# Kernel optimization log

Hardware: AMD Instinct MI355X
Metric: run time of the kernel (lower is better)

The kernel has to match this reference:

```python
import jax, jax.numpy as jnp
import numpy as np

B, CIN, H, W = 4, 128, 128, 128
CH = CIN // 2          # channels after transpose conv (= 64)
COUT = 64
N2 = (B * 2 * H * 2 * W) // 2  # active sites of x2 (half of fine grid)


def setup_inputs() -> dict:
    key = jax.random.key(0)
    ks = jax.random.split(key, 8)
    n = lambda k, s, sc=1.0: jax.random.normal(k, s, jnp.float32) * sc
    return {
        "x1": n(ks[0], (B, CIN, H, W)),
        "x2_feat": n(ks[1], (N2, CH)),
        "w_up": n(ks[2], (CIN, CH, 2, 2), 0.05),   # torch ConvTranspose2d layout [in, out, kh, kw]
        "b_up": n(ks[3], (CH,), 0.05),
        "w1": n(ks[4], (CH, CH, 3, 3), 0.05),      # torch Conv2d layout [out, in, kh, kw]
        "b1": n(ks[5], (CH,), 0.05),
        "a1": jnp.full((1,), 0.25, jnp.float32),   # nn.PReLU default init
        "w2": n(ks[6], (COUT, CH, 3, 3), 0.05),
        "b2": n(ks[7], (COUT,), 0.05),
        "a2": jnp.full((1,), 0.25, jnp.float32),
    }


def _prelu(x, a):
    return jnp.where(x >= 0, x, a * x)


def _conv3(x, w, b):
    y = jax.lax.conv_general_dilated(x, w, (1, 1), 'SAME',
                                     dimension_numbers=('NCHW', 'OIHW', 'NCHW'))
    return y + b[None, :, None, None]


def reference(x1, x2_feat, w_up, b_up, w1, b1, a1, w2, b2, a2):
    Bn, _, Hn, Wn = x1.shape
    # ConvTranspose2d k=2, s=2 (non-overlapping) as an einsum:
    # up[b,o,2i+p,2j+q] = sum_c x1[b,c,i,j] * w_up[c,o,p,q]
    up = jnp.einsum('bchw,copq->bohpwq', x1, w_up).reshape(Bn, CH, 2 * Hn, 2 * Wn)
    up = up + b_up[None, :, None, None]
    # addspvec: larger tensor keeps its indices; first len(b) feature rows
    # are overwritten by the smaller tensor's features (spconv raster order).
    f = jnp.transpose(up, (0, 2, 3, 1)).reshape(-1, CH)  # [B*2H*2W, CH]
    f = f.at[:x2_feat.shape[0]].set(x2_feat)
    merged = jnp.transpose(f.reshape(Bn, 2 * Hn, 2 * Wn, CH), (0, 3, 1, 2))
    # DoubleConv: (SparseConv2d 3x3 pad1 -> PReLU) x 2 (dense-equivalent)
    h = _prelu(_conv3(merged, w1, b1), a1[0])
    out = _prelu(_conv3(h, w2, b2), a2[0])
    return out
```

## Files before the change

### kernel.cpp

```cpp
#include <hip/hip_runtime.h>

typedef __attribute__((ext_vector_type(8))) short short8;
typedef __attribute__((ext_vector_type(4))) float f32x4;

#define HF 256
#define WF 256

typedef const __attribute__((address_space(1))) void gbl_void;
typedef __attribute__((address_space(3))) void lds_void;

__device__ __forceinline__ ushort f2bf(float f) {
    uint u = __builtin_bit_cast(uint, f);
    u = (u + 0x7FFFu + ((u >> 16) & 1u)) >> 16;
    return (ushort)u;
}
__device__ __forceinline__ uint pack2(float a, float b) {
    return (uint)f2bf(a) | ((uint)f2bf(b) << 16);
}
__device__ __forceinline__ float prelu(float v, float al) { return v >= 0.f ? v : al * v; }

__global__ __launch_bounds__(256) void k_wprep(const float* __restrict__ w1,
                                               const float* __restrict__ w2,
                                               const float* __restrict__ wup,
                                               ushort* __restrict__ wT1,
                                               ushort* __restrict__ wT2,
                                               ushort* __restrict__ wupT,
                                               uint4* __restrict__ zeroBuf) {
    int idx = blockIdx.x * 256 + threadIdx.x;
    if (blockIdx.x == 0 && threadIdx.x < 16)
        zeroBuf[threadIdx.x] = make_uint4(0u, 0u, 0u, 0u);
    if (idx < 36864) {
        int tap = idx >> 12;
        int oc  = idx & 4095;
        int src = oc * 9 + tap;
        wT1[idx] = f2bf(w1[src]);
        wT2[idx] = f2bf(w2[src]);
    }
    if (idx < 32768) {
        int out = idx >> 7;
        int c   = idx & 127;
        int k   = out >> 6;
        int o   = out & 63;
        wupT[idx] = f2bf(wup[c * 256 + o * 4 + k]);
    }
}

__global__ __launch_bounds__(512) void k_upsample_mfma(const float* __restrict__ x1,
                                                       const ushort* __restrict__ wupT,
                                                       const float* __restrict__ bup,
                                                       ushort* __restrict__ upB) {
    __shared__ __align__(16) char lds[81920];

    const int t   = threadIdx.x;
    const int l   = t & 63;
    const int l15 = l & 15;
    const int l4  = l >> 4;
    const int w   = t >> 6;
    const int pg  = w & 3;
    const int oh  = w >> 2;
    const int i   = blockIdx.x >> 1;
    const int j0  = (blockIdx.x & 1) * 64;
    const int z   = blockIdx.y;
    const int gb  = 2 + z;

    {
        const int j  = t & 63;
        const int cg = t >> 6;
        const size_t base = ((size_t)gb * 128) * 16384 + (size_t)i * 128 + j0 + j;
        float xv[16];
#pragma unroll
        for (int r = 0; r < 2; ++r)
#pragma unroll
            for (int cc = 0; cc < 8; ++cc)
                xv[r * 8 + cc] = x1[base + (size_t)(cg * 16 + r * 8 + cc) * 16384];
#pragma unroll
        for (int r = 0; r < 2; ++r) {
            short8 pk;
#pragma unroll
            for (int cc = 0; cc < 8; ++cc) pk[cc] = (short)f2bf(xv[r * 8 + cc]);
            int ad = (j * 256 + (cg * 16 + r * 8) * 2) ^ ((j & 15) << 4);
            *(short8*)(lds + ad) = pk;
        }
    }
    {
        const uint4* src = (const uint4*)wupT;
#pragma unroll
        for (int rep = 0; rep < 8; ++rep) {
            int q   = rep * 512 + t;
            int out = q >> 4, c16 = q & 15;
            int ad  = 16384 + ((out * 256 + c16 * 16) ^ ((out & 15) << 4));
            *(uint4*)(lds + ad) = src[q];
        }
    }
    float bvv[4];
#pragma unroll
    for (int ob = 0; ob < 4; ++ob) bvv[ob] = bup[ob * 16 + l15];
    __syncthreads();

    f32x4 acc[2][4];
#pragma unroll
    for (int kk = 0; kk < 2; ++kk)
#pragma unroll
        for (int ob = 0; ob < 4; ++ob) acc[kk][ob] = (f32x4){0.f, 0.f, 0.f, 0.f};

#pragma unroll
    for (int ks = 0; ks < 4; ++ks) {
        const int cb = ks * 64 + (l4 << 4);
        const int rowA = pg * 16 + l15;
        short8 xfr = *(const short8*)(lds + ((rowA * 256 + cb) ^ ((rowA & 15) << 4)));
#pragma unroll
        for (int kk = 0; kk < 2; ++kk)
#pragma unroll
            for (int ob = 0; ob < 4; ++ob) {
                int out = (oh * 2 + kk) * 64 + ob * 16 + l15;
                short8 wfr = *(const short8*)(lds + 16384 +
                              ((out * 256 + cb) ^ ((out & 15) << 4)));
                acc[kk][ob] = __builtin_amdgcn_mfma_f32_16x16x32_bf16(xfr, wfr, acc[kk][ob], 0, 0, 0);
            }
    }
    __syncthreads();

    ushort* OUT = (ushort*)lds;
#pragma unroll
    for (int kk = 0; kk < 2; ++kk) {
        const int k = oh * 2 + kk, p = k >> 1, q = k & 1;
#pragma unroll
        for (int ob = 0; ob < 4; ++ob) {
            const int o = ob * 16 + l15;
#pragma unroll
            for (int r = 0; r < 4; ++r) {
                int jl = pg * 16 + l4 * 4 + r;
                int x  = 2 * jl + q;
                OUT[(p * 128 + x) * 64 + o] = f2bf(acc[kk][ob][r] + bvv[ob]);
            }
        }
    }
    __syncthreads();

#pragma unroll
    for (int rep = 0; rep < 4; ++rep) {
        int idx = rep * 512 + t;
        int p   = idx >> 10;
        int y   = 2 * i + p;
        uint4 v = *(const uint4*)(lds + idx * 16);
        size_t g = (size_t)(z * HF + y) * 2048 + (size_t)j0 * 16 + (idx & 1023);
        ((uint4*)upB)[g] = v;
    }
}

template<int IN_MODE, int OUT_NHWC>
__global__ __launch_bounds__(1024, 1) void k_conv(const float* __restrict__ x2,
                                                  const ushort* __restrict__ upB,
                                                  const ushort* __restrict__ inB,
                                                  const ushort* __restrict__ wT,
                                                  const float* __restrict__ bias,
                                                  const float* __restrict__ alpha,
                                                  const uint4* __restrict__ zeroBuf,
                                                  ushort* __restrict__ outB,
                                                  float* __restrict__ outF) {
    __shared__ __align__(16) ushort inL[5120 * 8];
    __shared__ __align__(16) ushort wL[9 * 64 * 64];

    const int t   = threadIdx.x;
    const int wv  = t >> 6;
    const int l   = t & 63;
    const int l15 = l & 15;
    const int l4  = l >> 4;
    const int x0  = (blockIdx.x & 7) * 32;
    const int y0  = (blockIdx.x >> 3) * 16;
    const int b   = blockIdx.y;

    {
        const char* wTb = (const char*)wT;
#pragma unroll
        for (int rep = 0; rep < 4; ++rep) {
            int d   = rep * 1024 + t;
            int tap = d >> 9;
            int dp  = d & 511;
            int s   = (tap << 9) + (dp ^ ((dp >> 3) & 7));
            __builtin_amdgcn_global_load_lds(
                (gbl_void*)(wTb + (size_t)s * 16),
                (lds_void*)((char*)wL + (size_t)((rep << 10) + (wv << 6)) * 16),
                16, 0, 0);
        }
        if (wv < 8) {
            int d   = 4096 + (wv << 6) + l;
            int tap = d >> 9;
            int dp  = d & 511;
            int s   = (tap << 9) + (dp ^ ((dp >> 3) & 7));
            __builtin_amdgcn_global_load_lds(
                (gbl_void*)(wTb + (size_t)s * 16),
                (lds_void*)((char*)wL + (size_t)(4096 + (wv << 6)) * 16),
                16, 0, 0);
        }
    }

    if (IN_MODE == 1 || b >= 2) {
        const ushort* src0 = (IN_MODE == 1) ? inB : upB;
        const int bb = (IN_MODE == 1) ? b : (b - 2);
#pragma unroll
        for (int rep = 0; rep < 5; ++rep) {
            int d  = rep * 1024 + t;
            int r  = d / 272;
            int wi = d - r * 272;
            int wq = wi ^ ((wi >> 3) & 7);
            int x  = wq >> 3, c8 = wq & 7;
            int gy = y0 - 1 + r;
            int gx = x0 - 1 + x;
            const void* g;
            if (d < 4896 && (unsigned)gy < HF && (unsigned)gx < WF) {
                size_t pos = (size_t)(bb * HF + gy) * WF + gx;
                g = (const void*)(src0 + pos * 64 + c8 * 8);
            } else {
                g = (const void*)zeroBuf;
            }
            __builtin_amdgcn_global_load_lds(
                (gbl_void*)g,
                (lds_void*)((char*)inL + (size_t)((rep << 10) + (wv << 6)) * 16),
                16, 0, 0);
        }
    } else {
        for (int q = t; q < 18 * 34 * 8; q += 1024) {
            int r   = q / 272;
            int rem = q - r * 272;
            int x   = rem >> 3;
            int c8  = rem & 7;
            int gy = y0 - 1 + r;
            int gx = x0 - 1 + x;
            uint4 v = make_uint4(0u, 0u, 0u, 0u);
            if ((unsigned)gy < HF && (unsigned)gx < WF) {
                size_t pos = (size_t)(b * HF + gy) * WF + gx;
                const float4* s = (const float4*)(x2 + pos * 64 + c8 * 8);
                float4 u0 = s[0], u1 = s[1];
                v = make_uint4(pack2(u0.x, u0.y), pack2(u0.z, u0.w),
                               pack2(u1.x, u1.y), pack2(u1.z, u1.w));
            }
            int ad = (q * 16) ^ ((x & 7) << 4);
            *(uint4*)((char*)inL + ad) = v;
        }
    }
    __syncthreads();

    f32x4 acc[2][4];
#pragma unroll
    for (int m = 0; m < 2; ++m)
#pragma unroll
        for (int nf = 0; nf < 4; ++nf) acc[m][nf] = (f32x4){0.f, 0.f, 0.f, 0.f};

#pragma unroll 1
    for (int tap = 0; tap < 9; ++tap) {
        const int ky = tap / 3;
        const int kx = tap - ky * 3;
        const char* wPage = (const char*)wL + tap * 8192;
#pragma unroll
        for (int ks = 0; ks < 2; ++ks) {
            short8 wfr[4];
#pragma unroll
            for (int nf = 0; nf < 4; ++nf) {
                int o = nf * 16 + l15;
                int ad = (o * 128 + ks * 64 + (l4 << 4)) ^ ((o & 7) << 4);
                wfr[nf] = *(const short8*)(wPage + ad);
            }
#pragma unroll
            for (int m = 0; m < 2; ++m) {
                int ry = wv + ky;
                int xl = m * 16 + l15 + kx;
                int ad = ((ry * 34 + xl) * 128 + ks * 64 + (l4 << 4)) ^ ((xl & 7) << 4);
                short8 ifr = *(const short8*)((const char*)inL + ad);
#pragma unroll
                for (int nf = 0; nf < 4; ++nf) {
                    if (OUT_NHWC)
                        acc[m][nf] = __builtin_amdgcn_mfma_f32_16x16x32_bf16(
                            wfr[nf], ifr, acc[m][nf], 0, 0, 0);
                    else
                        acc[m][nf] = __builtin_amdgcn_mfma_f32_16x16x32_bf16(
                            ifr, wfr[nf], acc[m][nf], 0, 0, 0);
                }
            }
        }
    }

    const float al = alpha[0];
    const int y = y0 + wv;
    if (OUT_NHWC) {
        float4 bv[4];
#pragma unroll
        for (int nf = 0; nf < 4; ++nf) bv[nf] = *(const float4*)(bias + nf * 16 + (l4 << 2));
#pragma unroll
        for (int m = 0; m < 2; ++m) {
            int x = x0 + m * 16 + l15;
#pragma unroll
            for (int nf = 0; nf < 4; ++nf) {
                f32x4 v = acc[m][nf];
                uint lo = pack2(prelu(v.x + bv[nf].x, al), prelu(v.y + bv[nf].y, al));
                uint hi = pack2(prelu(v.z + bv[nf].z, al), prelu(v.w + bv[nf].w, al));
                int cb = nf * 16 + (l4 << 2);
                *(uint2*)(outB + ((size_t)(b * HF + y) * WF + x) * 64 + cb) = make_uint2(lo, hi);
            }
        }
    } else {
        float bb[4];
#pragma unroll
        for (int nf = 0; nf < 4; ++nf) bb[nf] = bias[nf * 16 + l15];
#pragma unroll
        for (int m = 0; m < 2; ++m) {
            int xb = x0 + m * 16 + (l4 << 2);
#pragma unroll
            for (int nf = 0; nf < 4; ++nf) {
                f32x4 v = acc[m][nf];
                int cout = nf * 16 + l15;
                float4 st;
                st.x = prelu(v.x + bb[nf], al);
                st.y = prelu(v.y + bb[nf], al);
                st.z = prelu(v.z + bb[nf], al);
                st.w = prelu(v.w + bb[nf], al);
                *(float4*)(outF + (((size_t)b * 64 + cout) << 16) + y * WF + xb) = st;
            }
        }
    }
}

extern "C" void kernel_launch(void* const* d_in, const int* in_sizes, int n_in,
                              void* d_out, int out_size, void* d_ws, size_t ws_size,
                              hipStream_t stream) {
    const float* x1  = (const float*)d_in[0];
    const float* x2  = (const float*)d_in[1];
    const float* wup = (const float*)d_in[2];
    const float* bup = (const float*)d_in[3];
    const float* w1  = (const float*)d_in[4];
    const float* b1  = (const float*)d_in[5];
    const float* a1  = (const float*)d_in[6];
    const float* w2  = (const float*)d_in[7];
    const float* b2  = (const float*)d_in[8];
    const float* a2  = (const float*)d_in[9];

    char* ws = (char*)d_ws;
    ushort* upB  = (ushort*)ws;
    ushort* hB   = (ushort*)(ws + (size_t)(16 << 20));
    ushort* wT1  = (ushort*)(ws + (size_t)(48 << 20));
    ushort* wT2  = wT1 + 9 * 64 * 64;
    ushort* wupT = wT2 + 9 * 64 * 64;
    uint4*  zeroBuf = (uint4*)(ws + (size_t)(49 << 20));
    float* out = (float*)d_out;

    k_wprep<<<144, 256, 0, stream>>>(w1, w2, wup, wT1, wT2, wupT, zeroBuf);
    k_upsample_mfma<<<dim3(256, 2), 512, 0, stream>>>(x1, wupT, bup, upB);
    k_conv<0, 1><<<dim3(128, 4), 1024, 0, stream>>>(x2, upB, nullptr, wT1, b1, a1, zeroBuf, hB, nullptr);
    k_conv<1, 0><<<dim3(128, 4), 1024, 0, stream>>>(nullptr, nullptr, hB, wT2, b2, a2, zeroBuf, nullptr, out);
}
```

Baseline: 80.10 us.

## Split conv K dimension across wave halves with LDS reduction

```diff
diff --git a/kernel.cpp b/kernel.cpp
--- a/kernel.cpp
+++ b/kernel.cpp
@@ -158,11 +158,15 @@
                                                   const uint4* __restrict__ zeroBuf,
                                                   ushort* __restrict__ outB,
                                                   float* __restrict__ outF) {
-    __shared__ __align__(16) ushort inL[5120 * 8];
-    __shared__ __align__(16) ushort wL[9 * 64 * 64];
+    __shared__ __align__(16) char ldsAll[155648];
+    ushort* inL = (ushort*)ldsAll;
+    ushort* wL  = (ushort*)(ldsAll + 81920);
+    float*  redL = (float*)ldsAll;
 
     const int t   = threadIdx.x;
     const int wv  = t >> 6;
+    const int wk  = wv & 7;
+    const int ks  = wv >> 3;
     const int l   = t & 63;
     const int l15 = l & 15;
     const int l4  = l >> 4;
@@ -241,80 +245,100 @@
     }
     __syncthreads();
 
-    f32x4 acc[2][4];
-#pragma unroll
-    for (int m = 0; m < 2; ++m)
+    f32x4 acc[4][4];
+#pragma unroll
+    for (int m = 0; m < 4; ++m)
 #pragma unroll
         for (int nf = 0; nf < 4; ++nf) acc[m][nf] = (f32x4){0.f, 0.f, 0.f, 0.f};
+
+    const int ksb = ks * 64 + (l4 << 4);
 
 #pragma unroll 1
     for (int tap = 0; tap < 9; ++tap) {
         const int ky = tap / 3;
         const int kx = tap - ky * 3;
         const char* wPage = (const char*)wL + tap * 8192;
-#pragma unroll
-        for (int ks = 0; ks < 2; ++ks) {
-            short8 wfr[4];
+        short8 wfr[4];
+#pragma unroll
+        for (int nf = 0; nf < 4; ++nf) {
+            int o = nf * 16 + l15;
+            int ad = (o * 128 + ksb) ^ ((o & 7) << 4);
+            wfr[nf] = *(const short8*)(wPage + ad);
+        }
+#pragma unroll
+        for (int m = 0; m < 4; ++m) {
+            int ry = wk * 2 + (m >> 1) + ky;
+            int xl = (m & 1) * 16 + l15 + kx;
+            int ad = ((ry * 34 + xl) * 128 + ksb) ^ ((xl & 7) << 4);
+            short8 ifr = *(const short8*)((const char*)inL + ad);
 #pragma unroll
             for (int nf = 0; nf < 4; ++nf) {
-                int o = nf * 16 + l15;
-                int ad = (o * 128 + ks * 64 + (l4 << 4)) ^ ((o & 7) << 4);
-                wfr[nf] = *(const short8*)(wPage + ad);
-            }
-#pragma unroll
-            for (int m = 0; m < 2; ++m) {
-                int ry = wv + ky;
-                int xl = m * 16 + l15 + kx;
-                int ad = ((ry * 34 + xl) * 128 + ks * 64 + (l4 << 4)) ^ ((xl & 7) << 4);
-                short8 ifr = *(const short8*)((const char*)inL + ad);
+                if (OUT_NHWC)
+                    acc[m][nf] = __builtin_amdgcn_mfma_f32_16x16x32_bf16(
+                        wfr[nf], ifr, acc[m][nf], 0, 0, 0);
+                else
+                    acc[m][nf] = __builtin_amdgcn_mfma_f32_16x16x32_bf16(
+                        ifr, wfr[nf], acc[m][nf], 0, 0, 0);
+            }
+        }
+    }
+
+    __syncthreads();
+    if (ks == 1) {
+#pragma unroll
+        for (int m = 0; m < 4; ++m)
+#pragma unroll
+            for (int nf = 0; nf < 4; ++nf)
+                *(f32x4*)(redL + (size_t)(((wk * 16 + m * 4 + nf) * 64 + l) * 4)) = acc[m][nf];
+    }
+    __syncthreads();
+    if (ks == 0) {
+        const float al = alpha[0];
+#pragma unroll
+        for (int m = 0; m < 4; ++m)
+#pragma unroll
+            for (int nf = 0; nf < 4; ++nf) {
+                f32x4 p = *(const f32x4*)(redL + (size_t)(((wk * 16 + m * 4 + nf) * 64 + l) * 4));
+                acc[m][nf].x += p.x; acc[m][nf].y += p.y;
+                acc[m][nf].z += p.z; acc[m][nf].w += p.w;
+            }
+        if (OUT_NHWC) {
+            float4 bv[4];
+#pragma unroll
+            for (int nf = 0; nf < 4; ++nf) bv[nf] = *(const float4*)(bias + nf * 16 + (l4 << 2));
+#pragma unroll
+            for (int m = 0; m < 4; ++m) {
+                int y = y0 + wk * 2 + (m >> 1);
+                int x = x0 + (m & 1) * 16 + l15;
 #pragma unroll
                 for (int nf = 0; nf < 4; ++nf) {
-                    if (OUT_NHWC)
-                        acc[m][nf] = __builtin_amdgcn_mfma_f32_16x16x32_bf16(
-                            wfr[nf], ifr, acc[m][nf], 0, 0, 0);
-                    else
-                        acc[m][nf] = __builtin_amdgcn_mfma_f32_16x16x32_bf16(
-                            ifr, wfr[nf], acc[m][nf], 0, 0, 0);
+                    f32x4 v = acc[m][nf];
+                    uint lo = pack2(prelu(v.x + bv[nf].x, al), prelu(v.y + bv[nf].y, al));
+                    uint hi = pack2(prelu(v.z + bv[nf].z, al), prelu(v.w + bv[nf].w, al));
+                    int cb = nf * 16 + (l4 << 2);
+                    *(uint2*)(outB + ((size_t)(b * HF + y) * WF + x) * 64 + cb) =
+                        make_uint2(lo, hi);
                 }
             }
-        }
-    }
-
-    const float al = alpha[0];
-    const int y = y0 + wv;
-    if (OUT_NHWC) {
-        float4 bv[4];
-#pragma unroll
-        for (int nf = 0; nf < 4; ++nf) bv[nf] = *(const float4*)(bias + nf * 16 + (l4 << 2));
-#pragma unroll
-        for (int m = 0; m < 2; ++m) {
-            int x = x0 + m * 16 + l15;
-#pragma unroll
-            for (int nf = 0; nf < 4; ++nf) {
-                f32x4 v = acc[m][nf];
-                uint lo = pack2(prelu(v.x + bv[nf].x, al), prelu(v.y + bv[nf].y, al));
-                uint hi = pack2(prelu(v.z + bv[nf].z, al), prelu(v.w + bv[nf].w, al));
-                int cb = nf * 16 + (l4 << 2);
-                *(uint2*)(outB + ((size_t)(b * HF + y) * WF + x) * 64 + cb) = make_uint2(lo, hi);
-            }
-        }
-    } else {
-        float bb[4];
-#pragma unroll
-        for (int nf = 0; nf < 4; ++nf) bb[nf] = bias[nf * 16 + l15];
-#pragma unroll
-        for (int m = 0; m < 2; ++m) {
-            int xb = x0 + m * 16 + (l4 << 2);
-#pragma unroll
-            for (int nf = 0; nf < 4; ++nf) {
-                f32x4 v = acc[m][nf];
-                int cout = nf * 16 + l15;
-                float4 st;
-                st.x = prelu(v.x + bb[nf], al);
-                st.y = prelu(v.y + bb[nf], al);
-                st.z = prelu(v.z + bb[nf], al);
-                st.w = prelu(v.w + bb[nf], al);
-                *(float4*)(outF + (((size_t)b * 64 + cout) << 16) + y * WF + xb) = st;
+        } else {
+            float bb[4];
+#pragma unroll
+            for (int nf = 0; nf < 4; ++nf) bb[nf] = bias[nf * 16 + l15];
+#pragma unroll
+            for (int m = 0; m < 4; ++m) {
+                int y  = y0 + wk * 2 + (m >> 1);
+                int xb = x0 + (m & 1) * 16 + (l4 << 2);
+#pragma unroll
+                for (int nf = 0; nf < 4; ++nf) {
+                    f32x4 v = acc[m][nf];
+                    int cout = nf * 16 + l15;
+                    float4 st;
+                    st.x = prelu(v.x + bb[nf], al);
+                    st.y = prelu(v.y + bb[nf], al);
+                    st.z = prelu(v.z + bb[nf], al);
+                    st.w = prelu(v.w + bb[nf], al);
+                    *(float4*)(outF + (((size_t)b * 64 + cout) << 16) + y * WF + xb) = st;
+                }
             }
         }
     }
```

Measured after the change: 87.59 us. +9.4%, slower.
